# Performance work log

Hardware: AMD Instinct MI355X
Metric: run time of the kernel (lower is better)

## Reference

```python
import jax, jax.numpy as jnp
import numpy as np
import math

N_EMBD = 1024
N_HEAD = 16
HEAD_DIM = N_EMBD // N_HEAD
SCALE = 1.0 / math.sqrt(HEAD_DIM)


def setup_inputs() -> dict:
    key = jax.random.key(0)
    ks = jax.random.split(key, 5)
    B, S = 1, 4096
    std = 0.02
    x = jax.random.normal(ks[0], (B, S, N_EMBD), dtype=jnp.float32)
    # Linear weights stored as [in, out] (transposed vs torch storage; same math)
    w_qkv = jax.random.normal(ks[1], (N_EMBD, 3 * N_EMBD), dtype=jnp.float32) * std
    b_qkv = jnp.zeros((3 * N_EMBD,), dtype=jnp.float32)
    w_out = jax.random.normal(ks[2], (N_EMBD, N_EMBD), dtype=jnp.float32) * std
    b_out = jnp.zeros((N_EMBD,), dtype=jnp.float32)
    return {"x": x, "w_qkv": w_qkv, "b_qkv": b_qkv, "w_out": w_out, "b_out": b_out}


def reference(x, w_qkv, b_qkv, w_out, b_out):
    B, S, D = x.shape
    qkv = x @ w_qkv + b_qkv                      # [B, S, 3D]
    q, k, v = jnp.split(qkv, 3, axis=-1)
    # [B, H, S, d]
    q = q.reshape(B, S, N_HEAD, HEAD_DIM).transpose(0, 2, 1, 3)
    k = k.reshape(B, S, N_HEAD, HEAD_DIM).transpose(0, 2, 1, 3)
    v = v.reshape(B, S, N_HEAD, HEAD_DIM).transpose(0, 2, 1, 3)
    scores = jnp.einsum("bhqd,bhkd->bhqk", q, k) * SCALE  # [B, H, S, S]
    causal = jnp.tril(jnp.ones((S, S), dtype=bool))
    scores = jnp.where(causal, scores, -jnp.inf)
    attn = jax.nn.softmax(scores, axis=-1)
    out = jnp.einsum("bhqk,bhkd->bhqd", attn, v)  # [B, H, S, d]
    out = out.transpose(0, 2, 1, 3).reshape(B, S, D)
    return out @ w_out + b_out
```

## Files before the change

kernel.cpp:

```cpp
#include <hip/hip_runtime.h>
#include <hip/hip_bf16.h>
#include <cstdint>

typedef __bf16 bf16x8 __attribute__((ext_vector_type(8)));
typedef float  f32x4  __attribute__((ext_vector_type(4)));

#define S_LEN 4096
#define D_EMB 1024
#define N3    3072
#define HDIM  64

__device__ __forceinline__ unsigned short f2bf(float f) {
    union { unsigned int i; float f; } v; v.f = f;
    unsigned int i = v.i;
    return (unsigned short)((i + 0x7FFFu + ((i >> 16) & 1u)) >> 16);
}

__device__ __forceinline__ void async16(const void* g, void* l) {
    __builtin_amdgcn_global_load_lds(
        (const __attribute__((address_space(1))) unsigned int*)g,
        (__attribute__((address_space(3))) unsigned int*)l,
        16, 0, 0);
}

__global__ void convert_f32_bf16(const float* __restrict__ src,
                                 unsigned short* __restrict__ dst, int n8) {
    const int i = blockIdx.x * blockDim.x + threadIdx.x;
    if (i >= n8) return;
    float4 f0 = *(const float4*)&src[i * 8];
    float4 f1 = *(const float4*)&src[i * 8 + 4];
    union { uint4 q; unsigned short s[8]; } o;
    o.s[0]=f2bf(f0.x); o.s[1]=f2bf(f0.y); o.s[2]=f2bf(f0.z); o.s[3]=f2bf(f0.w);
    o.s[4]=f2bf(f1.x); o.s[5]=f2bf(f1.y); o.s[6]=f2bf(f1.z); o.s[7]=f2bf(f1.w);
    *(uint4*)&dst[i * 8] = o.q;
}

__global__ void transpose_f32_to_bf16(const float* __restrict__ src,
                                      unsigned short* __restrict__ dst,
                                      int R, int ld, int c0) {
    __shared__ float tile[32][33];
    const int tx = threadIdx.x, ty = threadIdx.y;
    const int r0 = blockIdx.y * 32, cc0 = blockIdx.x * 32;
    for (int i = 0; i < 32; i += 8)
        tile[ty + i][tx] = src[(size_t)(r0 + ty + i) * ld + c0 + cc0 + tx];
    __syncthreads();
    for (int i = 0; i < 32; i += 8)
        dst[(size_t)(cc0 + ty + i) * R + r0 + tx] = f2bf(tile[tx][ty + i]);
}

__global__ void transpose_bf16(const unsigned short* __restrict__ src,
                               unsigned short* __restrict__ dst,
                               int R, int ld, int c0) {
    __shared__ unsigned short tile[32][33];
    const int tx = threadIdx.x, ty = threadIdx.y;
    const int r0 = blockIdx.y * 32, cc0 = blockIdx.x * 32;
    for (int i = 0; i < 32; i += 8)
        tile[ty + i][tx] = src[(size_t)(r0 + ty + i) * ld + c0 + cc0 + tx];
    __syncthreads();
    for (int i = 0; i < 32; i += 8)
        dst[(size_t)(cc0 + ty + i) * R + r0 + tx] = tile[tx][ty + i];
}

template <bool OUT_F32>
__global__ __launch_bounds__(256) void gemm_bt_bias(
    const unsigned short* __restrict__ A,
    const unsigned short* __restrict__ BT,
    const float* __restrict__ bias,
    void* __restrict__ Cp,
    int M, int N, int K)
{
    __shared__ __align__(16) unsigned short As[128 * 32];
    __shared__ __align__(16) unsigned short Bs[128 * 32];
    const int tid  = threadIdx.x;
    const int wave = tid >> 6, lane = tid & 63;
    const int q4 = lane >> 4, l16 = lane & 15;
    const int m0 = blockIdx.y * 128, n0 = blockIdx.x * 128;
    const int wm = (wave >> 1) * 64, wn = (wave & 1) * 64;

    f32x4 acc[4][4] = {};

    const int srow = wave * 32 + (lane >> 2);
    const int scol = (lane & 3) * 8;

    for (int k0 = 0; k0 < K; k0 += 32) {
        __syncthreads();
        for (int i = 0; i < 2; ++i) {
            const int r = srow + i * 16;
            async16(A  + (size_t)(m0 + r) * K + k0 + scol,
                    &As[(wave * 32 + i * 16) * 32 + lane * 8]);
            async16(BT + (size_t)(n0 + r) * K + k0 + scol,
                    &Bs[(wave * 32 + i * 16) * 32 + lane * 8]);
        }
        __syncthreads();

        bf16x8 af[4], bfr[4];
        for (int mi = 0; mi < 4; ++mi)
            af[mi] = *(const bf16x8*)&As[(wm + mi * 16 + l16) * 32 + q4 * 8];
        for (int ni = 0; ni < 4; ++ni)
            bfr[ni] = *(const bf16x8*)&Bs[(wn + ni * 16 + l16) * 32 + q4 * 8];
        for (int mi = 0; mi < 4; ++mi)
            for (int ni = 0; ni < 4; ++ni)
                acc[mi][ni] = __builtin_amdgcn_mfma_f32_16x16x32_bf16(
                    af[mi], bfr[ni], acc[mi][ni], 0, 0, 0);
    }

    for (int ni = 0; ni < 4; ++ni) {
        const int col = n0 + wn + ni * 16 + l16;
        const float bv = bias[col];
        for (int mi = 0; mi < 4; ++mi) {
            const int row = m0 + wm + mi * 16 + q4 * 4;
            for (int r = 0; r < 4; ++r) {
                const float val = acc[mi][ni][r] + bv;
                if constexpr (OUT_F32)
                    ((float*)Cp)[(size_t)(row + r) * N + col] = val;
                else
                    ((unsigned short*)Cp)[(size_t)(row + r) * N + col] = f2bf(val);
            }
        }
    }
}

#define LDP 72
__global__ __launch_bounds__(256) void attn_flash(
    const unsigned short* __restrict__ qkv,
    const unsigned short* __restrict__ Vt,
    unsigned short* __restrict__ X2)
{
    __shared__ __align__(16) unsigned short Ks[64 * LDP];
    __shared__ __align__(16) unsigned short Vs[64 * LDP];
    __shared__ __align__(16) unsigned short Ps[4 * 16 * LDP];
    const int tid  = threadIdx.x;
    const int wave = tid >> 6, lane = tid & 63;
    const int q4 = lane >> 4, l16 = lane & 15;
    const int h  = blockIdx.y;

    const int x = blockIdx.x, hg = blockIdx.y >> 2;
    int qt;
    if      (hg == 0) qt = x;
    else if (hg == 1) qt = 63 - x;
    else if (hg == 2) qt = (x + 16) & 63;
    else              qt = (47 - x) & 63;
    const int q0 = qt * 64;

    bf16x8 aq[2];
    {
        const unsigned short* qp =
            qkv + (size_t)(q0 + wave * 16 + l16) * N3 + h * HDIM + q4 * 8;
        aq[0] = *(const bf16x8*)(qp);
        aq[1] = *(const bf16x8*)(qp + 32);
    }

    float l_part = 0.f;
    f32x4 o[4] = {};

    const int rr = tid >> 3;
    const int cc = (tid & 7) * 8;
    const int ntile = qt + 1;
    const int grow = q0 + wave * 16 + l16;

    uint4 kv_a, kv_b, vt_a, vt_b;
    {
        kv_a = *(const uint4*)&qkv[(size_t)(rr)      * N3 + D_EMB + h * HDIM + cc];
        kv_b = *(const uint4*)&qkv[(size_t)(32 + rr) * N3 + D_EMB + h * HDIM + cc];
        vt_a = *(const uint4*)&Vt [(size_t)(h * HDIM + rr)      * S_LEN + cc];
        vt_b = *(const uint4*)&Vt [(size_t)(h * HDIM + 32 + rr) * S_LEN + cc];
    }

    for (int t = 0; t < ntile; ++t) {
        const int kv0 = t * 64;
        __syncthreads();
        *(uint4*)&Ks[rr * LDP + cc]        = kv_a;
        *(uint4*)&Ks[(32 + rr) * LDP + cc] = kv_b;
        *(uint4*)&Vs[rr * LDP + cc]        = vt_a;
        *(uint4*)&Vs[(32 + rr) * LDP + cc] = vt_b;
        if (t + 1 < ntile) {
            const int kn = kv0 + 64;
            kv_a = *(const uint4*)&qkv[(size_t)(kn + rr)      * N3 + D_EMB + h * HDIM + cc];
            kv_b = *(const uint4*)&qkv[(size_t)(kn + 32 + rr) * N3 + D_EMB + h * HDIM + cc];
            vt_a = *(const uint4*)&Vt [(size_t)(h * HDIM + rr)      * S_LEN + kn + cc];
            vt_b = *(const uint4*)&Vt [(size_t)(h * HDIM + 32 + rr) * S_LEN + kn + cc];
        }
        __syncthreads();

        f32x4 sacc[4] = {};
        for (int kk = 0; kk < 2; ++kk)
            for (int nt = 0; nt < 4; ++nt) {
                bf16x8 kf = *(const bf16x8*)&Ks[(nt * 16 + l16) * LDP + kk * 32 + q4 * 8];
                sacc[nt] = __builtin_amdgcn_mfma_f32_16x16x32_bf16(
                    kf, aq[kk], sacc[nt], 0, 0, 0);
            }

        const bool lastt = (t == ntile - 1);
        for (int nt = 0; nt < 4; ++nt) {
            float e[4];
            for (int r = 0; r < 4; ++r) {
                e[r] = __expf(sacc[nt][r] * 0.125f);
                if (lastt && (kv0 + nt * 16 + q4 * 4 + r > grow)) e[r] = 0.f;
                l_part += e[r];
            }
            union { uint2 q; unsigned short s[4]; } pk;
            pk.s[0] = f2bf(e[0]); pk.s[1] = f2bf(e[1]);
            pk.s[2] = f2bf(e[2]); pk.s[3] = f2bf(e[3]);
            *(uint2*)&Ps[wave * 16 * LDP + l16 * LDP + nt * 16 + q4 * 4] = pk.q;
        }
        __asm__ volatile("s_waitcnt lgkmcnt(0)" ::: "memory");

        for (int kk = 0; kk < 2; ++kk) {
            bf16x8 pa = *(const bf16x8*)&Ps[wave * 16 * LDP + l16 * LDP + kk * 32 + q4 * 8];
            for (int dt = 0; dt < 4; ++dt) {
                bf16x8 vb = *(const bf16x8*)&Vs[(dt * 16 + l16) * LDP + kk * 32 + q4 * 8];
                o[dt] = __builtin_amdgcn_mfma_f32_16x16x32_bf16(pa, vb, o[dt], 0, 0, 0);
            }
        }
    }

    float l = l_part;
    l += __shfl_xor(l, 16);
    l += __shfl_xor(l, 32);
    float linv[4];
    for (int r = 0; r < 4; ++r)
        linv[r] = 1.f / __shfl(l, q4 * 4 + r);

    for (int dt = 0; dt < 4; ++dt)
        for (int r = 0; r < 4; ++r) {
            const int row = q0 + wave * 16 + q4 * 4 + r;
            X2[(size_t)row * D_EMB + h * HDIM + dt * 16 + l16] =
                f2bf(o[dt][r] * linv[r]);
        }
}

extern "C" void kernel_launch(void* const* d_in, const int* in_sizes, int n_in,
                              void* d_out, int out_size, void* d_ws, size_t ws_size,
                              hipStream_t stream) {
    const float* x     = (const float*)d_in[0];
    const float* w_qkv = (const float*)d_in[1];
    const float* b_qkv = (const float*)d_in[2];
    const float* w_out = (const float*)d_in[3];
    const float* b_out = (const float*)d_in[4];
    float* out = (float*)d_out;

    char* ws = (char*)d_ws;
    unsigned short* qkv   = (unsigned short*)(ws);
    unsigned short* wqkvT = (unsigned short*)(ws + 25165824);
    unsigned short* woutT = (unsigned short*)(ws + 31457280);
    unsigned short* Vt    = (unsigned short*)(ws + 33554432);
    unsigned short* X2    = (unsigned short*)(ws + 41943040);
    unsigned short* Xb    = X2;

    convert_f32_bf16<<<(4096 * 1024 / 8 + 255) / 256, 256, 0, stream>>>(
        x, Xb, 4096 * 1024 / 8);

    transpose_f32_to_bf16<<<dim3(3072 / 32, 1024 / 32), dim3(32, 8), 0, stream>>>(
        w_qkv, wqkvT, 1024, 3072, 0);
    transpose_f32_to_bf16<<<dim3(1024 / 32, 1024 / 32), dim3(32, 8), 0, stream>>>(
        w_out, woutT, 1024, 1024, 0);

    gemm_bt_bias<false><<<dim3(3072 / 128, 4096 / 128), 256, 0, stream>>>(
        Xb, wqkvT, b_qkv, qkv, 4096, 3072, 1024);

    transpose_bf16<<<dim3(1024 / 32, 4096 / 32), dim3(32, 8), 0, stream>>>(
        qkv, Vt, 4096, 3072, 2048);

    attn_flash<<<dim3(64, 16), 256, 0, stream>>>(qkv, Vt, X2);

    gemm_bt_bias<true><<<dim3(1024 / 128, 4096 / 128), 256, 0, stream>>>(
        X2, woutT, b_out, out, 4096, 1024, 1024);
}
```

Measured before the change: 225.3 us.

## Double attention query tile to 128 rows per block, two subtiles per wave

Each block now handles 128 query rows (32 per wave, as two 16-row subtiles), so every K/V tile staged in LDS and every K/V fragment loaded into registers serves twice as many MFMAs. The grid halves to 32x16 and the load-balancing permutation becomes a simple two-way reversal. Waves whose rows sit entirely before the current KV tile skip compute, and masking is limited to diagonal tiles. The trade-offs are more register pressure, fewer blocks in flight, and some waves idling on the causal diagonal.

After: 262.5 us. 16.5% more time.

```diff
diff --git a/kernel.cpp b/kernel.cpp
--- a/kernel.cpp
+++ b/kernel.cpp
@@ -128,35 +128,32 @@
 {
     __shared__ __align__(16) unsigned short Ks[64 * LDP];
     __shared__ __align__(16) unsigned short Vs[64 * LDP];
-    __shared__ __align__(16) unsigned short Ps[4 * 16 * LDP];
+    __shared__ __align__(16) unsigned short Ps[8 * 16 * LDP];
     const int tid  = threadIdx.x;
     const int wave = tid >> 6, lane = tid & 63;
     const int q4 = lane >> 4, l16 = lane & 15;
     const int h  = blockIdx.y;
 
-    const int x = blockIdx.x, hg = blockIdx.y >> 2;
-    int qt;
-    if      (hg == 0) qt = x;
-    else if (hg == 1) qt = 63 - x;
-    else if (hg == 2) qt = (x + 16) & 63;
-    else              qt = (47 - x) & 63;
-    const int q0 = qt * 64;
-
-    bf16x8 aq[2];
-    {
+    const int x = blockIdx.x, hg = blockIdx.y >> 3;
+    const int qt = hg ? (31 - x) : x;
+    const int q0 = qt * 128;
+    const int wbase = q0 + wave * 32;
+
+    bf16x8 aq[2][2];
+#pragma unroll
+    for (int s = 0; s < 2; ++s) {
         const unsigned short* qp =
-            qkv + (size_t)(q0 + wave * 16 + l16) * N3 + h * HDIM + q4 * 8;
-        aq[0] = *(const bf16x8*)(qp);
-        aq[1] = *(const bf16x8*)(qp + 32);
-    }
-
-    float l_part = 0.f;
-    f32x4 o[4] = {};
+            qkv + (size_t)(wbase + s * 16 + l16) * N3 + h * HDIM + q4 * 8;
+        aq[s][0] = *(const bf16x8*)(qp);
+        aq[s][1] = *(const bf16x8*)(qp + 32);
+    }
+
+    float l_part[2] = {0.f, 0.f};
+    f32x4 o[2][4] = {};
 
     const int rr = tid >> 3;
     const int cc = (tid & 7) * 8;
-    const int ntile = qt + 1;
-    const int grow = q0 + wave * 16 + l16;
+    const int ntile = 2 * qt + 2;
 
     uint4 kv_a, kv_b, vt_a, vt_b;
     {
@@ -182,51 +179,87 @@
         }
         __syncthreads();
 
-        f32x4 sacc[4] = {};
+        if (kv0 > wbase + 31) continue;
+
+        f32x4 sacc[2][4] = {};
+#pragma unroll
+        for (int kk = 0; kk < 2; ++kk) {
+            bf16x8 kf[4];
+#pragma unroll
+            for (int nt = 0; nt < 4; ++nt)
+                kf[nt] = *(const bf16x8*)&Ks[(nt * 16 + l16) * LDP + kk * 32 + q4 * 8];
+#pragma unroll
+            for (int s = 0; s < 2; ++s)
+#pragma unroll
+                for (int nt = 0; nt < 4; ++nt)
+                    sacc[s][nt] = __builtin_amdgcn_mfma_f32_16x16x32_bf16(
+                        kf[nt], aq[s][kk], sacc[s][nt], 0, 0, 0);
+        }
+
+        bf16x8 vb[2][4];
+#pragma unroll
         for (int kk = 0; kk < 2; ++kk)
+#pragma unroll
+            for (int dt = 0; dt < 4; ++dt)
+                vb[kk][dt] = *(const bf16x8*)&Vs[(dt * 16 + l16) * LDP + kk * 32 + q4 * 8];
+
+        bool sact[2];
+#pragma unroll
+        for (int s = 0; s < 2; ++s) {
+            sact[s] = (kv0 <= wbase + s * 16 + 15);
+            if (!sact[s]) continue;
+            const int grow = wbase + s * 16 + l16;
+            const bool maskt = (kv0 + 63 > wbase + s * 16);
+#pragma unroll
             for (int nt = 0; nt < 4; ++nt) {
-                bf16x8 kf = *(const bf16x8*)&Ks[(nt * 16 + l16) * LDP + kk * 32 + q4 * 8];
-                sacc[nt] = __builtin_amdgcn_mfma_f32_16x16x32_bf16(
-                    kf, aq[kk], sacc[nt], 0, 0, 0);
+                float e[4];
+#pragma unroll
+                for (int r = 0; r < 4; ++r) {
+                    e[r] = __expf(sacc[s][nt][r] * 0.125f);
+                    if (maskt && (kv0 + nt * 16 + q4 * 4 + r > grow)) e[r] = 0.f;
+                    l_part[s] += e[r];
+                }
+                union { uint2 q; unsigned short w[4]; } pk;
+                pk.w[0] = f2bf(e[0]); pk.w[1] = f2bf(e[1]);
+                pk.w[2] = f2bf(e[2]); pk.w[3] = f2bf(e[3]);
+                *(uint2*)&Ps[((wave * 2 + s) * 16 + l16) * LDP + nt * 16 + q4 * 4] = pk.q;
             }
-
-        const bool lastt = (t == ntile - 1);
-        for (int nt = 0; nt < 4; ++nt) {
-            float e[4];
+        }
+        __asm__ volatile("s_waitcnt lgkmcnt(0)" ::: "memory");
+
+#pragma unroll
+        for (int s = 0; s < 2; ++s) {
+            if (!sact[s]) continue;
+#pragma unroll
+            for (int kk = 0; kk < 2; ++kk) {
+                bf16x8 pa = *(const bf16x8*)
+                    &Ps[((wave * 2 + s) * 16 + l16) * LDP + kk * 32 + q4 * 8];
+#pragma unroll
+                for (int dt = 0; dt < 4; ++dt)
+                    o[s][dt] = __builtin_amdgcn_mfma_f32_16x16x32_bf16(
+                        pa, vb[kk][dt], o[s][dt], 0, 0, 0);
+            }
+        }
+    }
+
+#pragma unroll
+    for (int s = 0; s < 2; ++s) {
+        float l = l_part[s];
+        l += __shfl_xor(l, 16);
+        l += __shfl_xor(l, 32);
+        float linv[4];
+#pragma unroll
+        for (int r = 0; r < 4; ++r)
+            linv[r] = 1.f / __shfl(l, q4 * 4 + r);
+#pragma unroll
+        for (int dt = 0; dt < 4; ++dt)
+#pragma unroll
             for (int r = 0; r < 4; ++r) {
-                e[r] = __expf(sacc[nt][r] * 0.125f);
-                if (lastt && (kv0 + nt * 16 + q4 * 4 + r > grow)) e[r] = 0.f;
-                l_part += e[r];
+                const int row = wbase + s * 16 + q4 * 4 + r;
+                X2[(size_t)row * D_EMB + h * HDIM + dt * 16 + l16] =
+                    f2bf(o[s][dt][r] * linv[s == 0 ? r : r]);
             }
-            union { uint2 q; unsigned short s[4]; } pk;
-            pk.s[0] = f2bf(e[0]); pk.s[1] = f2bf(e[1]);
-            pk.s[2] = f2bf(e[2]); pk.s[3] = f2bf(e[3]);
-            *(uint2*)&Ps[wave * 16 * LDP + l16 * LDP + nt * 16 + q4 * 4] = pk.q;
-        }
-        __asm__ volatile("s_waitcnt lgkmcnt(0)" ::: "memory");
-
-        for (int kk = 0; kk < 2; ++kk) {
-            bf16x8 pa = *(const bf16x8*)&Ps[wave * 16 * LDP + l16 * LDP + kk * 32 + q4 * 8];
-            for (int dt = 0; dt < 4; ++dt) {
-                bf16x8 vb = *(const bf16x8*)&Vs[(dt * 16 + l16) * LDP + kk * 32 + q4 * 8];
-                o[dt] = __builtin_amdgcn_mfma_f32_16x16x32_bf16(pa, vb, o[dt], 0, 0, 0);
-            }
-        }
-    }
-
-    float l = l_part;
-    l += __shfl_xor(l, 16);
-    l += __shfl_xor(l, 32);
-    float linv[4];
-    for (int r = 0; r < 4; ++r)
-        linv[r] = 1.f / __shfl(l, q4 * 4 + r);
-
-    for (int dt = 0; dt < 4; ++dt)
-        for (int r = 0; r < 4; ++r) {
-            const int row = q0 + wave * 16 + q4 * 4 + r;
-            X2[(size_t)row * D_EMB + h * HDIM + dt * 16 + l16] =
-                f2bf(o[dt][r] * linv[r]);
-        }
+    }
 }
 
 extern "C" void kernel_launch(void* const* d_in, const int* in_sizes, int n_in,
@@ -261,7 +294,7 @@
     transpose_bf16<<<dim3(1024 / 32, 4096 / 32), dim3(32, 8), 0, stream>>>(
         qkv, Vt, 4096, 3072, 2048);
 
-    attn_flash<<<dim3(64, 16), 256, 0, stream>>>(qkv, Vt, X2);
+    attn_flash<<<dim3(32, 16), 256, 0, stream>>>(qkv, Vt, X2);
 
     gemm_bt_bias<true><<<dim3(1024 / 128, 4096 / 128), 256, 0, stream>>>(
         X2, woutT, b_out, out, 4096, 1024, 1024);
```
